# Kernel tuning notes

Measured on AMD Instinct MI355X. Metric: run time of the kernel, lower is better.

The kernel has to match this reference:

```python
import jax, jax.numpy as jnp
import numpy as np

N_NODES = 50000
N_EDGES = 800000
N_GRAPHS = 64
FEAT = 125
POS = 3
CONV = 256
LIN = 256
OUT = 10


def _glorot(key, shape):
    fan_in, fan_out = shape[1], shape[0]
    lim = jnp.sqrt(6.0 / (fan_in + fan_out))
    return jax.random.uniform(key, shape, jnp.float32, -lim, lim)


def setup_inputs() -> dict:
    key = jax.random.key(0)
    ks = jax.random.split(key, 16)
    x = jax.random.normal(ks[0], (N_NODES, FEAT), jnp.float32)
    pos = jax.random.normal(ks[1], (N_NODES, POS), jnp.float32)
    edge_index = jax.random.randint(ks[2], (2, N_EDGES), 0, N_NODES, jnp.int64)
    batch = jnp.sort(jax.random.randint(ks[3], (N_NODES,), 0, N_GRAPHS, jnp.int64))
    in0 = FEAT + POS  # 128
    inp = {
        'x': x, 'pos': pos, 'edge_index': edge_index, 'batch': batch,
        'Wl0': _glorot(ks[4], (CONV, in0)), 'bl0': jnp.zeros((CONV,), jnp.float32), 'Wr0': _glorot(ks[5], (CONV, in0)),
        'Wl1': _glorot(ks[6], (CONV, CONV)), 'bl1': jnp.zeros((CONV,), jnp.float32), 'Wr1': _glorot(ks[7], (CONV, CONV)),
        'Wl2': _glorot(ks[8], (CONV, CONV)), 'bl2': jnp.zeros((CONV,), jnp.float32), 'Wr2': _glorot(ks[9], (CONV, CONV)),
        'lin_W': _glorot(ks[10], (LIN, CONV)), 'lin_b': jnp.zeros((LIN,), jnp.float32),
        'out_W': _glorot(ks[11], (OUT, LIN)), 'out_b': jnp.zeros((OUT,), jnp.float32),
    }
    return inp


def _sage_conv(x, src, dst, Wl, bl, Wr):
    # PyG SAGEConv (aggr='mean'): out = lin_l(mean_{j in N(i)} x_j) + lin_r(x_i)
    n = x.shape[0]
    s = jax.ops.segment_sum(x[src], dst, num_segments=n)            # [N, F]
    cnt = jax.ops.segment_sum(jnp.ones((src.shape[0], 1), x.dtype), dst, num_segments=n)
    agg = s / jnp.maximum(cnt, 1.0)
    return agg @ Wl.T + bl + x @ Wr.T


def reference(x, pos, edge_index, batch, Wl0, bl0, Wr0, Wl1, bl1, Wr1,
              Wl2, bl2, Wr2, lin_W, lin_b, out_W, out_b):
    src, dst = edge_index[0], edge_index[1]
    h = jnp.concatenate([x, pos], axis=1)                           # [N, 128]
    for Wl, bl, Wr in ((Wl0, bl0, Wr0), (Wl1, bl1, Wr1), (Wl2, bl2, Wr2)):
        h = jax.nn.relu(_sage_conv(h, src, dst, Wl, bl, Wr))
    g = jax.ops.segment_max(h, batch, num_segments=N_GRAPHS)        # [G, 256] global_max_pool
    g = g @ lin_W.T + lin_b
    return g @ out_W.T + out_b                                      # [G, 10]
```

## Files before the change

kernel.cpp:

```cpp
#include <hip/hip_runtime.h>
#include <hip/hip_bf16.h>

#define N_NODES 50000
#define N_EDGES 800000
#define N_GRAPHS 64
#define SCAN_BLK 98

typedef __attribute__((ext_vector_type(8))) short bf16x8;
typedef __attribute__((ext_vector_type(4))) float f32x4;

__device__ __forceinline__ float bf2f(ushort u) { return __uint_as_float(((unsigned)u) << 16); }
__device__ __forceinline__ ushort f2bf(float f) {
    unsigned b = __float_as_uint(f);
    b += 0x7fffu + ((b >> 16) & 1u);
    return (ushort)(b >> 16);
}

__global__ void build_h0(const float* __restrict__ x, const float* __restrict__ pos,
                         ushort* __restrict__ h0, int n) {
    const size_t total = (size_t)n * 128;
    for (size_t idx = (size_t)blockIdx.x * blockDim.x + threadIdx.x; idx < total;
         idx += (size_t)gridDim.x * blockDim.x) {
        int i = (int)(idx >> 7);
        int j = (int)(idx & 127);
        float v = (j < 125) ? x[(size_t)i * 125 + j] : pos[(size_t)i * 3 + (j - 125)];
        h0[idx] = f2bf(v);
    }
}

__global__ void convert_weights(const float* __restrict__ w0, const float* __restrict__ w1,
                                const float* __restrict__ w2, const float* __restrict__ w3,
                                const float* __restrict__ w4, const float* __restrict__ w5,
                                ushort* __restrict__ o) {
    const int total = 32768 * 2 + 65536 * 4;
    for (int i = blockIdx.x * blockDim.x + threadIdx.x; i < total; i += gridDim.x * blockDim.x) {
        float v;
        if (i < 32768) v = w0[i];
        else if (i < 65536) v = w1[i - 32768];
        else {
            int j = i - 65536;
            int m = j >> 16;
            int r = j & 65535;
            v = (m == 0) ? w2[r] : (m == 1) ? w3[r] : (m == 2) ? w4[r] : w5[r];
        }
        o[i] = f2bf(v);
    }
}

__global__ void hist_dst(const int* __restrict__ dst, int* __restrict__ deg, int e) {
    for (int i = blockIdx.x * blockDim.x + threadIdx.x; i < e; i += gridDim.x * blockDim.x)
        atomicAdd(&deg[dst[i]], 1);
}

__global__ __launch_bounds__(256) void scan_k1(const int* __restrict__ deg,
                                               int* __restrict__ bsum, int n) {
    const int b = blockIdx.x, t = threadIdx.x;
    const int j = b * 512 + t * 2;
    int x = (j < n) ? deg[j] : 0;
    int y = (j + 1 < n) ? deg[j + 1] : 0;
    __shared__ int sm[256];
    sm[t] = x + y;
    __syncthreads();
    for (int st = 1; st < 256; st <<= 1) {
        int v = (t >= st) ? sm[t - st] : 0;
        __syncthreads();
        sm[t] += v;
        __syncthreads();
    }
    if (t == 255) bsum[b] = sm[255];
}

__global__ __launch_bounds__(128) void scan_k2(const int* __restrict__ bsum,
                                               int* __restrict__ bpre, int* __restrict__ off_n,
                                               int nb) {
    const int t = threadIdx.x;
    const int v = (t < nb) ? bsum[t] : 0;
    __shared__ int sm[128];
    sm[t] = v;
    __syncthreads();
    for (int st = 1; st < 128; st <<= 1) {
        int u = (t >= st) ? sm[t - st] : 0;
        __syncthreads();
        sm[t] += u;
        __syncthreads();
    }
    if (t < nb) bpre[t] = sm[t] - v;
    if (t == 127) off_n[0] = sm[127];
}

__global__ __launch_bounds__(256) void scan_k3(const int* __restrict__ deg,
                                               const int* __restrict__ bpre,
                                               int* __restrict__ off, int* __restrict__ cur,
                                               int n) {
    const int b = blockIdx.x, t = threadIdx.x;
    const int j = b * 512 + t * 2;
    int x = (j < n) ? deg[j] : 0;
    int y = (j + 1 < n) ? deg[j + 1] : 0;
    const int s = x + y;
    __shared__ int sm[256];
    sm[t] = s;
    __syncthreads();
    for (int st = 1; st < 256; st <<= 1) {
        int u = (t >= st) ? sm[t - st] : 0;
        __syncthreads();
        sm[t] += u;
        __syncthreads();
    }
    const int v0 = bpre[b] + sm[t] - s;
    if (j < n) { off[j] = v0; cur[j] = v0; }
    if (j + 1 < n) { off[j + 1] = v0 + x; cur[j + 1] = v0 + x; }
}

__global__ void fill_csr(const int* __restrict__ src, const int* __restrict__ dst,
                         int* __restrict__ cur, ushort* __restrict__ csr, int e) {
    for (int i = blockIdx.x * blockDim.x + threadIdx.x; i < e; i += gridDim.x * blockDim.x) {
        int pos = atomicAdd(&cur[dst[i]], 1);
        csr[pos] = (ushort)src[i];
    }
}

template <int F>
__global__ __launch_bounds__(256) void csr_mean(const ushort* __restrict__ h,
                                                const int* __restrict__ off,
                                                const ushort* __restrict__ idx,
                                                ushort* __restrict__ s, int n) {
    const int node = blockIdx.x * 4 + (threadIdx.x >> 6);
    if (node >= n) return;
    const int lane = threadIdx.x & 63;
    constexpr int LPR = F / 8;
    constexpr int EPW = 64 / LPR;
    const int sub = lane / LPR;
    const int l = lane % LPR;
    const int b = off[node];
    const int cnt = off[node + 1] - b;

    float s0[8] = {}, s1[8] = {}, s2[8] = {}, s3[8] = {};
    const ushort* hl = h + (size_t)l * 8;
    int q = sub;
    for (; q + 3 * EPW < cnt; q += 4 * EPW) {
        int i0 = idx[b + q];
        int i1 = idx[b + q + EPW];
        int i2 = idx[b + q + 2 * EPW];
        int i3 = idx[b + q + 3 * EPW];
        bf16x8 v0 = *(const bf16x8*)(hl + (size_t)i0 * F);
        bf16x8 v1 = *(const bf16x8*)(hl + (size_t)i1 * F);
        bf16x8 v2 = *(const bf16x8*)(hl + (size_t)i2 * F);
        bf16x8 v3 = *(const bf16x8*)(hl + (size_t)i3 * F);
#pragma unroll
        for (int j = 0; j < 8; ++j) s0[j] += bf2f((ushort)v0[j]);
#pragma unroll
        for (int j = 0; j < 8; ++j) s1[j] += bf2f((ushort)v1[j]);
#pragma unroll
        for (int j = 0; j < 8; ++j) s2[j] += bf2f((ushort)v2[j]);
#pragma unroll
        for (int j = 0; j < 8; ++j) s3[j] += bf2f((ushort)v3[j]);
    }
    for (; q < cnt; q += EPW) {
        int i0 = idx[b + q];
        bf16x8 v0 = *(const bf16x8*)(hl + (size_t)i0 * F);
#pragma unroll
        for (int j = 0; j < 8; ++j) s0[j] += bf2f((ushort)v0[j]);
    }
    const float w = 1.0f / (float)max(cnt, 1);
    bf16x8 o;
#pragma unroll
    for (int j = 0; j < 8; ++j) {
        float a = (s0[j] + s1[j]) + (s2[j] + s3[j]);
        if constexpr (EPW == 4) a += __shfl_xor(a, 16);
        a += __shfl_xor(a, 32);
        o[j] = (short)f2bf(a * w);
    }
    if (sub == 0) *(bf16x8*)(s + (size_t)node * F + l * 8) = o;
}

__global__ __launch_bounds__(256, 3) void sage_gemm(
    const ushort* __restrict__ S, const ushort* __restrict__ H,
    const ushort* __restrict__ Wl, const ushort* __restrict__ Wr,
    const float* __restrict__ bias, ushort* __restrict__ O, int n, int F) {
    constexpr int BM = 128, BN = 128, BK = 64;
    constexpr int LDK = BK + 8;
    __shared__ ushort As[BM * LDK];
    __shared__ ushort Bs[BN * LDK];
    const int row0 = blockIdx.x * BM;
    const int col0 = blockIdx.y * BN;
    const int tid = threadIdx.x;
    const int wid = tid >> 6;
    const int wr = wid >> 1;
    const int wc = wid & 1;
    const int lane = tid & 63;
    const int lr = lane & 15;
    const int lk = lane >> 4;

    f32x4 acc[4][4] = {};

    const int Ktot = 2 * F;
    for (int kb = 0; kb < Ktot; kb += BK) {
        const bool left = (kb < F);
        const int kofs = left ? kb : kb - F;
        const ushort* __restrict__ Ab = left ? S : H;
        const ushort* __restrict__ Wb = left ? Wl : Wr;
#pragma unroll
        for (int p = 0; p < 4; ++p) {
            const int c = tid + p * 256;
            const int r = c >> 3;
            const int kc = (c & 7) * 8;
            const int gr = min(row0 + r, n - 1);
            bf16x8 va = *(const bf16x8*)(Ab + (size_t)gr * F + kofs + kc);
            *(bf16x8*)(&As[r * LDK + kc]) = va;
            bf16x8 vb = *(const bf16x8*)(Wb + (size_t)(col0 + r) * F + kofs + kc);
            *(bf16x8*)(&Bs[r * LDK + kc]) = vb;
        }
        __syncthreads();
#pragma unroll
        for (int kh = 0; kh < 2; ++kh) {
            bf16x8 af[4], bg[4];
#pragma unroll
            for (int m = 0; m < 4; ++m)
                af[m] = *(const bf16x8*)&As[(wr * 64 + m * 16 + lr) * LDK + kh * 32 + lk * 8];
#pragma unroll
            for (int q = 0; q < 4; ++q)
                bg[q] = *(const bf16x8*)&Bs[(wc * 64 + q * 16 + lr) * LDK + kh * 32 + lk * 8];
#pragma unroll
            for (int m = 0; m < 4; ++m)
#pragma unroll
                for (int q = 0; q < 4; ++q)
                    acc[m][q] =
                        __builtin_amdgcn_mfma_f32_16x16x32_bf16(af[m], bg[q], acc[m][q], 0, 0, 0);
        }
        __syncthreads();
    }
#pragma unroll
    for (int q = 0; q < 4; ++q) {
        const int col = col0 + wc * 64 + q * 16 + lr;
        const float bv = bias[col];
#pragma unroll
        for (int m = 0; m < 4; ++m) {
            const int row = row0 + wr * 64 + m * 16 + lk * 4;
#pragma unroll
            for (int j = 0; j < 4; ++j) {
                if (row + j < n)
                    O[(size_t)(row + j) * 256 + col] = f2bf(fmaxf(acc[m][q][j] + bv, 0.f));
            }
        }
    }
}

__global__ __launch_bounds__(256) void pool_max(const ushort* __restrict__ h,
                                                const int* __restrict__ batch,
                                                int* __restrict__ gpool, int n) {
    const int CHUNK = 32;
    const int wave = threadIdx.x >> 6;
    const int lane = threadIdx.x & 63;
    const int c0 = (blockIdx.x * 4 + wave) * CHUNK;
    if (c0 >= n) return;
    const int c1 = min(c0 + CHUNK, n);
    const int fb = lane * 4;
    float m0 = 0.f, m1 = 0.f, m2 = 0.f, m3 = 0.f;
    int g = batch[c0];
    for (int i = c0; i < c1; ++i) {
        const int bg = batch[i];
        if (bg != g) {
            int* gp = &gpool[g * 256 + fb];
            atomicMax(gp + 0, __float_as_int(m0));
            atomicMax(gp + 1, __float_as_int(m1));
            atomicMax(gp + 2, __float_as_int(m2));
            atomicMax(gp + 3, __float_as_int(m3));
            m0 = m1 = m2 = m3 = 0.f;
            g = bg;
        }
        const ushort4 v = *(const ushort4*)(h + (size_t)i * 256 + fb);
        m0 = fmaxf(m0, bf2f(v.x));
        m1 = fmaxf(m1, bf2f(v.y));
        m2 = fmaxf(m2, bf2f(v.z));
        m3 = fmaxf(m3, bf2f(v.w));
    }
    int* gp = &gpool[g * 256 + fb];
    atomicMax(gp + 0, __float_as_int(m0));
    atomicMax(gp + 1, __float_as_int(m1));
    atomicMax(gp + 2, __float_as_int(m2));
    atomicMax(gp + 3, __float_as_int(m3));
}

__global__ __launch_bounds__(256) void head_kernel(
    const float* __restrict__ gpool, const float* __restrict__ linW,
    const float* __restrict__ linb, const float* __restrict__ outW,
    const float* __restrict__ outb, float* __restrict__ out) {
    __shared__ float gin[256];
    __shared__ float gl[256];
    int g = blockIdx.x, t = threadIdx.x;
    gin[t] = gpool[g * 256 + t];
    __syncthreads();
    float acc = linb[t];
    const float* w = linW + (size_t)t * 256;
#pragma unroll 4
    for (int k = 0; k < 256; ++k) acc = fmaf(gin[k], w[k], acc);
    gl[t] = acc;
    __syncthreads();
    if (t < 160) {
        int o = t >> 4, s = t & 15;
        float p = 0.f;
        for (int k = s; k < 256; k += 16) p = fmaf(gl[k], outW[o * 256 + k], p);
        p += __shfl_down(p, 8, 16);
        p += __shfl_down(p, 4, 16);
        p += __shfl_down(p, 2, 16);
        p += __shfl_down(p, 1, 16);
        if (s == 0) out[g * 10 + o] = p + outb[o];
    }
}

extern "C" void kernel_launch(void* const* d_in, const int* in_sizes, int n_in,
                              void* d_out, int out_size, void* d_ws, size_t ws_size,
                              hipStream_t stream) {
    const float* x    = (const float*)d_in[0];
    const float* pos  = (const float*)d_in[1];
    const int* ei     = (const int*)d_in[2];
    const int* batch  = (const int*)d_in[3];
    const float* Wl0  = (const float*)d_in[4];
    const float* bl0  = (const float*)d_in[5];
    const float* Wr0  = (const float*)d_in[6];
    const float* Wl1  = (const float*)d_in[7];
    const float* bl1  = (const float*)d_in[8];
    const float* Wr1  = (const float*)d_in[9];
    const float* Wl2  = (const float*)d_in[10];
    const float* bl2  = (const float*)d_in[11];
    const float* Wr2  = (const float*)d_in[12];
    const float* linW = (const float*)d_in[13];
    const float* linb = (const float*)d_in[14];
    const float* outW = (const float*)d_in[15];
    const float* outb = (const float*)d_in[16];
    float* out = (float*)d_out;

    const int* src = ei;
    const int* dst = ei + N_EDGES;
    const int N = N_NODES, E = N_EDGES;

    ushort* hA   = (ushort*)d_ws;
    ushort* hB   = hA + (size_t)N * 256;
    ushort* Sg   = hB + (size_t)N * 256;
    ushort* Wb   = Sg + (size_t)N * 256;
    int* off     = (int*)(Wb + 327680);
    int* cur     = off + (N + 1);
    ushort* csr  = (ushort*)(cur + N);
    int* gpool   = (int*)(csr + E);
    int* deg     = gpool + 64 * 256;
    int* bsum    = deg + N;
    int* bpre    = bsum + 128;

    ushort* Wl0b = Wb;
    ushort* Wr0b = Wb + 32768;
    ushort* Wl1b = Wb + 65536;
    ushort* Wr1b = Wb + 65536 + 65536;
    ushort* Wl2b = Wb + 65536 + 2 * 65536;
    ushort* Wr2b = Wb + 65536 + 3 * 65536;

    build_h0<<<dim3(1024), dim3(256), 0, stream>>>(x, pos, hA, N);
    convert_weights<<<dim3(640), dim3(256), 0, stream>>>(Wl0, Wr0, Wl1, Wr1, Wl2, Wr2, Wb);

    hipMemsetAsync(deg, 0, (size_t)N * sizeof(int), stream);
    hist_dst<<<dim3(1024), dim3(256), 0, stream>>>(dst, deg, E);
    scan_k1<<<dim3(SCAN_BLK), dim3(256), 0, stream>>>(deg, bsum, N);
    scan_k2<<<dim3(1), dim3(128), 0, stream>>>(bsum, bpre, off + N, SCAN_BLK);
    scan_k3<<<dim3(SCAN_BLK), dim3(256), 0, stream>>>(deg, bpre, off, cur, N);
    fill_csr<<<dim3(1024), dim3(256), 0, stream>>>(src, dst, cur, csr, E);

    const dim3 gemm_grid((N + 127) / 128, 2), blk(256);

    csr_mean<128><<<dim3((N + 3) / 4), blk, 0, stream>>>(hA, off, csr, Sg, N);
    sage_gemm<<<gemm_grid, blk, 0, stream>>>(Sg, hA, Wl0b, Wr0b, bl0, hB, N, 128);

    csr_mean<256><<<dim3((N + 3) / 4), blk, 0, stream>>>(hB, off, csr, Sg, N);
    sage_gemm<<<gemm_grid, blk, 0, stream>>>(Sg, hB, Wl1b, Wr1b, bl1, hA, N, 256);

    csr_mean<256><<<dim3((N + 3) / 4), blk, 0, stream>>>(hA, off, csr, Sg, N);
    sage_gemm<<<gemm_grid, blk, 0, stream>>>(Sg, hA, Wl2b, Wr2b, bl2, hB, N, 256);

    hipMemsetAsync(gpool, 0, (size_t)N_GRAPHS * 256 * sizeof(int), stream);
    pool_max<<<dim3((N + 127) / 128), blk, 0, stream>>>(hB, batch, gpool, N);
    head_kernel<<<dim3(N_GRAPHS), blk, 0, stream>>>((const float*)gpool, linW, linb, outW, outb,
                                                    out);
}
```

Before: 378.4 us.

## Use direct global-to-LDS loads with XOR swizzle in GEMM; partition CSR fill by destination

The GEMM tile loads now use global_load_lds, which writes 16-byte chunks straight into LDS without passing through registers. The padded LDS layout is replaced by an XOR swizzle on the k-group so that MFMA fragment reads stay free of bank conflicts. Separately, fill_csr splits its blocks into 8 groups, and each group scans every edge but only handles destinations in its own node range. This aims to localise the atomics and cut cache contention, at the cost of reading dst eight times.

Result: faster. 369.3 us (-2.4%).

```diff
diff --git a/kernel.cpp b/kernel.cpp
--- a/kernel.cpp
+++ b/kernel.cpp
@@ -8,12 +8,19 @@
 
 typedef __attribute__((ext_vector_type(8))) short bf16x8;
 typedef __attribute__((ext_vector_type(4))) float f32x4;
+
+#define AS1 __attribute__((address_space(1)))
+#define AS3 __attribute__((address_space(3)))
 
 __device__ __forceinline__ float bf2f(ushort u) { return __uint_as_float(((unsigned)u) << 16); }
 __device__ __forceinline__ ushort f2bf(float f) {
     unsigned b = __float_as_uint(f);
     b += 0x7fffu + ((b >> 16) & 1u);
     return (ushort)(b >> 16);
+}
+
+__device__ __forceinline__ void gl_lds16(const ushort* g, ushort* l) {
+    __builtin_amdgcn_global_load_lds((const AS1 void*)g, (AS3 void*)l, 16, 0, 0);
 }
 
 __global__ void build_h0(const float* __restrict__ x, const float* __restrict__ pos,
@@ -111,11 +118,20 @@
     if (j + 1 < n) { off[j + 1] = v0 + x; cur[j + 1] = v0 + x; }
 }
 
-__global__ void fill_csr(const int* __restrict__ src, const int* __restrict__ dst,
-                         int* __restrict__ cur, ushort* __restrict__ csr, int e) {
-    for (int i = blockIdx.x * blockDim.x + threadIdx.x; i < e; i += gridDim.x * blockDim.x) {
-        int pos = atomicAdd(&cur[dst[i]], 1);
-        csr[pos] = (ushort)src[i];
+__global__ __launch_bounds__(256) void fill_csr(const int* __restrict__ src,
+                                                const int* __restrict__ dst,
+                                                int* __restrict__ cur,
+                                                ushort* __restrict__ csr, int e) {
+    const int g = blockIdx.x & 7;
+    const int bid = blockIdx.x >> 3;
+    const int nb = gridDim.x >> 3;
+    const int lo = g * (N_NODES / 8), hi = lo + (N_NODES / 8);
+    for (int i = bid * blockDim.x + threadIdx.x; i < e; i += nb * blockDim.x) {
+        const int d = dst[i];
+        if (d >= lo && d < hi) {
+            int pos = atomicAdd(&cur[d], 1);
+            csr[pos] = (ushort)src[i];
+        }
     }
 }
 
@@ -178,9 +194,8 @@
     const ushort* __restrict__ Wl, const ushort* __restrict__ Wr,
     const float* __restrict__ bias, ushort* __restrict__ O, int n, int F) {
     constexpr int BM = 128, BN = 128, BK = 64;
-    constexpr int LDK = BK + 8;
-    __shared__ ushort As[BM * LDK];
-    __shared__ ushort Bs[BN * LDK];
+    __shared__ ushort As[BM * BK];
+    __shared__ ushort Bs[BN * BK];
     const int row0 = blockIdx.x * BM;
     const int col0 = blockIdx.y * BN;
     const int tid = threadIdx.x;
@@ -190,6 +205,8 @@
     const int lane = tid & 63;
     const int lr = lane & 15;
     const int lk = lane >> 4;
+    const int lrow = lane >> 3;
+    const int lgg = lane & 7;
 
     f32x4 acc[4][4] = {};
 
@@ -201,25 +218,28 @@
         const ushort* __restrict__ Wb = left ? Wl : Wr;
 #pragma unroll
         for (int p = 0; p < 4; ++p) {
-            const int c = tid + p * 256;
-            const int r = c >> 3;
-            const int kc = (c & 7) * 8;
+            const int rb = (p * 4 + wid) * 8;
+            const int r = rb + lrow;
+            const int sg = (lgg ^ (r & 7)) << 3;
             const int gr = min(row0 + r, n - 1);
-            bf16x8 va = *(const bf16x8*)(Ab + (size_t)gr * F + kofs + kc);
-            *(bf16x8*)(&As[r * LDK + kc]) = va;
-            bf16x8 vb = *(const bf16x8*)(Wb + (size_t)(col0 + r) * F + kofs + kc);
-            *(bf16x8*)(&Bs[r * LDK + kc]) = vb;
+            gl_lds16(Ab + (size_t)gr * F + kofs + sg, &As[rb * 64]);
+            gl_lds16(Wb + (size_t)(col0 + r) * F + kofs + sg, &Bs[rb * 64]);
         }
         __syncthreads();
 #pragma unroll
         for (int kh = 0; kh < 2; ++kh) {
             bf16x8 af[4], bg[4];
-#pragma unroll
-            for (int m = 0; m < 4; ++m)
-                af[m] = *(const bf16x8*)&As[(wr * 64 + m * 16 + lr) * LDK + kh * 32 + lk * 8];
-#pragma unroll
-            for (int q = 0; q < 4; ++q)
-                bg[q] = *(const bf16x8*)&Bs[(wc * 64 + q * 16 + lr) * LDK + kh * 32 + lk * 8];
+            const int g = kh * 4 + lk;
+#pragma unroll
+            for (int m = 0; m < 4; ++m) {
+                const int ra = wr * 64 + m * 16 + lr;
+                af[m] = *(const bf16x8*)&As[ra * 64 + ((g ^ (ra & 7)) << 3)];
+            }
+#pragma unroll
+            for (int q = 0; q < 4; ++q) {
+                const int rb2 = wc * 64 + q * 16 + lr;
+                bg[q] = *(const bf16x8*)&Bs[rb2 * 64 + ((g ^ (rb2 & 7)) << 3)];
+            }
 #pragma unroll
             for (int m = 0; m < 4; ++m)
 #pragma unroll
@@ -361,7 +381,7 @@
     scan_k1<<<dim3(SCAN_BLK), dim3(256), 0, stream>>>(deg, bsum, N);
     scan_k2<<<dim3(1), dim3(128), 0, stream>>>(bsum, bpre, off + N, SCAN_BLK);
     scan_k3<<<dim3(SCAN_BLK), dim3(256), 0, stream>>>(deg, bpre, off, cur, N);
-    fill_csr<<<dim3(1024), dim3(256), 0, stream>>>(src, dst, cur, csr, E);
+    fill_csr<<<dim3(768), dim3(256), 0, stream>>>(src, dst, cur, csr, E);
 
     const dim3 gemm_grid((N + 127) / 128, 2), blk(256);
 
```
